# Optimization experiments

Hardware: AMD Instinct MI355X
Metric: run time of the kernel (lower is better)

## Reference

```python
import jax, jax.numpy as jnp
import numpy as np

D_MODEL = 1024
N_HEADS = 16
HEAD_DIM = D_MODEL // N_HEADS  # 64
TOP_K = 64
EPS = 1e-12  # matches F.normalize eps


def setup_inputs() -> dict:
    key = jax.random.key(0)
    ks = jax.random.split(key, 6)
    s = 0.02
    def w(k):
        return jax.random.normal(k, (D_MODEL, D_MODEL), jnp.float32) * s
    zb = jnp.zeros((D_MODEL,), jnp.float32)
    # x: (B, T, d_model); T must equal d_model (see compress_proj constraint)
    x = jax.random.normal(ks[0], (2, 1024, D_MODEL), jnp.float32)
    return {
        "x": x,
        "Wq": w(ks[1]), "bq": zb,
        "Wk": w(ks[2]), "bk": zb,
        "Wv": w(ks[3]), "bv": zb,
        "Wo": w(ks[4]), "bo": zb,
        "Wc": w(ks[5]), "bc": zb,  # compress_proj (applied along time axis)
    }


def _l2norm(a):
    n = jnp.linalg.norm(a, axis=-1, keepdims=True)
    return a / jnp.maximum(n, EPS)


def reference(x, Wq, bq, Wk, bk, Wv, bv, Wo, bo, Wc, bc):
    B, T, Dm = x.shape
    H, hd = N_HEADS, HEAD_DIM

    def proj(W, b):
        return (x @ W.T + b).reshape(B, T, H, hd).transpose(0, 2, 1, 3)  # (B,H,T,hd)

    Q = proj(Wq, bq)
    K = proj(Wk, bk)
    V = proj(Wv, bv)

    # compress_kv with compress_ratio=1: compress_proj acts on the (transposed)
    # time axis, so K_comp[b,h,c,d] = sum_t K[b,h,t,d] * Wc[c,t] + bc[c]
    K_comp = jnp.einsum('bhtd,ct->bhcd', K, Wc) + bc[None, None, :, None]
    V_comp = jnp.einsum('bhtd,ct->bhcd', V, Wc) + bc[None, None, :, None]

    # lightning indexer: cosine similarity + top-k over compressed slots
    sim = jnp.einsum('bhtd,bhcd->bhtc', _l2norm(Q), _l2norm(K_comp))
    topk_idx = jax.lax.top_k(sim, TOP_K)[1]  # (B,H,T,K)

    bi = jnp.arange(B)[:, None, None, None]
    hi = jnp.arange(H)[None, :, None, None]
    K_sel = K_comp[bi, hi, topk_idx]  # (B,H,T,K,hd)
    V_sel = V_comp[bi, hi, topk_idx]

    scores = jnp.einsum('bhtd,bhtkd->bhtk', Q, K_sel) / float(np.sqrt(hd))
    attn = jax.nn.softmax(scores, axis=-1)
    out = jnp.einsum('bhtk,bhtkd->bhtd', attn, V_sel)  # (B,H,T,hd)
    out = out.transpose(0, 2, 1, 3).reshape(B, T, Dm)
    return out @ Wo.T + bo
```

## Files before the change

kernel.cpp:

```cpp
#include <hip/hip_runtime.h>
#include <type_traits>


#define DEVI __device__ __forceinline__

constexpr int Tn = 1024;
constexpr int Cn = 1024;
constexpr int Hn = 16;

typedef short bf16x8 __attribute__((ext_vector_type(8)));
typedef float f32x4 __attribute__((ext_vector_type(4)));

DEVI int wsumi(int v)   { for (int m = 1; m < 64; m <<= 1) v += __shfl_xor(v, m); return v; }
DEVI int wmini(int v)   { for (int m = 1; m < 64; m <<= 1) { int o = __shfl_xor(v, m); v = o < v ? o : v; } return v; }
DEVI float wfmax(float v){ for (int m = 1; m < 64; m <<= 1) v = fmaxf(v, __shfl_xor(v, m)); return v; }
DEVI float wfsum(float v){ for (int m = 1; m < 64; m <<= 1) v += __shfl_xor(v, m); return v; }

DEVI unsigned long long mapd(double x) {
  unsigned long long b = (unsigned long long)__double_as_longlong(x);
  return (b >> 63) ? ~b : (b | 0x8000000000000000ull);
}

DEVI unsigned short f2bf_rne(float x) {
  unsigned u = __float_as_uint(x);
  u += 0x7fffu + ((u >> 16) & 1u);
  return (unsigned short)(u >> 16);
}
struct BfPair { short hi, lo; };
DEVI BfPair split2(float x) {
  unsigned short h = f2bf_rne(x);
  float hf = __uint_as_float(((unsigned)h) << 16);
  BfPair r;
  r.hi = (short)h;
  r.lo = (short)f2bf_rne(x - hf);
  return r;
}

template <typename OUTT, typename ACCT, bool BTRANS, int BIASMODE, bool SIM>
__global__ __launch_bounds__(256) void gemm_k(
    const float* __restrict__ A, const float* __restrict__ B,
    const float* __restrict__ bias, OUTT* __restrict__ C,
    int Kd, int lda, int ldb, int ldc,
    long long zA, long long zB, long long zC, int group_base)
{
  __shared__ float As[16][68];
  __shared__ float Bs[16][68];

  size_t offA, offB, offC;
  if (SIM) {
    int pair = group_base + (int)blockIdx.z;
    int bb = pair >> 4, hh = pair & 15;
    offA = ((size_t)bb * Tn) * (size_t)lda + (size_t)hh * 64;
    offB = ((size_t)bb * Cn) * (size_t)ldb + (size_t)hh * 64;
    offC = (size_t)blockIdx.z * (size_t)Tn * (size_t)ldc;
  } else {
    offA = (size_t)blockIdx.z * (size_t)zA;
    offB = (size_t)blockIdx.z * (size_t)zB;
    offC = (size_t)blockIdx.z * (size_t)zC;
  }
  const float* Ab = A + offA;
  const float* Bb = B + offB;
  OUTT* Cb = C + offC;

  const int tid = threadIdx.x;
  const int tx = tid & 15, ty = tid >> 4;
  const int m0 = blockIdx.y * 64, n0 = blockIdx.x * 64;

  ACCT acc[4][4];
#pragma unroll
  for (int i = 0; i < 4; ++i)
#pragma unroll
    for (int j = 0; j < 4; ++j) acc[i][j] = (ACCT)0;

  for (int k0 = 0; k0 < Kd; k0 += 16) {
    {
      int m = tid >> 2, kf = tid & 3;
      float4 a = *(const float4*)(Ab + (size_t)(m0 + m) * lda + k0 + 4 * kf);
      As[4 * kf + 0][m] = a.x; As[4 * kf + 1][m] = a.y;
      As[4 * kf + 2][m] = a.z; As[4 * kf + 3][m] = a.w;
    }
    if (BTRANS) {
      int n = tid >> 2, kf = tid & 3;
      float4 b = *(const float4*)(Bb + (size_t)(n0 + n) * ldb + k0 + 4 * kf);
      Bs[4 * kf + 0][n] = b.x; Bs[4 * kf + 1][n] = b.y;
      Bs[4 * kf + 2][n] = b.z; Bs[4 * kf + 3][n] = b.w;
    } else {
      int k = tid >> 4, nf = tid & 15;
      float4 b = *(const float4*)(Bb + (size_t)(k0 + k) * ldb + n0 + 4 * nf);
      *(float4*)&Bs[k][4 * nf] = b;
    }
    __syncthreads();
#pragma unroll
    for (int k = 0; k < 16; ++k) {
      float4 a4 = *(const float4*)&As[k][4 * ty];
      float4 b4 = *(const float4*)&Bs[k][4 * tx];
      float av[4] = {a4.x, a4.y, a4.z, a4.w};
      float bv[4] = {b4.x, b4.y, b4.z, b4.w};
#pragma unroll
      for (int i = 0; i < 4; ++i)
#pragma unroll
        for (int j = 0; j < 4; ++j)
          acc[i][j] += (ACCT)av[i] * (ACCT)bv[j];
    }
    __syncthreads();
  }

  if constexpr (std::is_same<OUTT, double>::value) {
#pragma unroll
    for (int i = 0; i < 4; ++i) {
      size_t m = (size_t)(m0 + 4 * ty + i);
      double* p = (double*)Cb + m * ldc + n0 + 4 * tx;
      p[0] = (double)acc[i][0]; p[1] = (double)acc[i][1];
      p[2] = (double)acc[i][2]; p[3] = (double)acc[i][3];
    }
  } else {
    float cbv[4] = {0.f, 0.f, 0.f, 0.f};
    if (BIASMODE == 1) {
      float4 b4 = *(const float4*)(bias + n0 + 4 * tx);
      cbv[0] = b4.x; cbv[1] = b4.y; cbv[2] = b4.z; cbv[3] = b4.w;
    }
#pragma unroll
    for (int i = 0; i < 4; ++i) {
      int m = m0 + 4 * ty + i;
      float rb = (BIASMODE == 2) ? bias[m] : 0.f;
      float4 s;
      s.x = (float)acc[i][0] + cbv[0] + rb;
      s.y = (float)acc[i][1] + cbv[1] + rb;
      s.z = (float)acc[i][2] + cbv[2] + rb;
      s.w = (float)acc[i][3] + cbv[3] + rb;
      *(float4*)((float*)Cb + (size_t)m * ldc + n0 + 4 * tx) = s;
    }
  }
}

template <bool BTRANS, int BIASMODE>
__global__ __launch_bounds__(256) void mfma_gemm_k(
    const float* __restrict__ A, const float* __restrict__ B,
    const float* __restrict__ bias, float* __restrict__ C,
    int Kd, int lda, int ldb, int ldc, long long zB, long long zC)
{
  __shared__ short Ah[4 * 64 * 8];
  __shared__ short Al[4 * 64 * 8];
  __shared__ short Bh[4 * 64 * 8];
  __shared__ short Bl[4 * 64 * 8];

  const float* Bz = B + (size_t)blockIdx.z * (size_t)zB;
  float* Cz = C + (size_t)blockIdx.z * (size_t)zC;

  const int tid = threadIdx.x;
  const int lane = tid & 63, w = tid >> 6;
  const int wr = w >> 1, wc = w & 1;
  const int m0 = blockIdx.y * 64, n0 = blockIdx.x * 64;
  const int r16 = lane & 15, kg = lane >> 4;

  f32x4 acc[2][2];
#pragma unroll
  for (int i = 0; i < 2; ++i)
#pragma unroll
    for (int j = 0; j < 2; ++j) acc[i][j] = (f32x4){0.f, 0.f, 0.f, 0.f};

  for (int k0 = 0; k0 < Kd; k0 += 32) {
    {
      int row = tid >> 2, kseg = tid & 3;
      const float* p = A + (size_t)(m0 + row) * lda + k0 + kseg * 8;
      float4 v0 = *(const float4*)p;
      float4 v1 = *(const float4*)(p + 4);
      BfPair q0 = split2(v0.x), q1 = split2(v0.y), q2 = split2(v0.z), q3 = split2(v0.w);
      BfPair q4 = split2(v1.x), q5 = split2(v1.y), q6 = split2(v1.z), q7 = split2(v1.w);
      bf16x8 h = {q0.hi, q1.hi, q2.hi, q3.hi, q4.hi, q5.hi, q6.hi, q7.hi};
      bf16x8 l = {q0.lo, q1.lo, q2.lo, q3.lo, q4.lo, q5.lo, q6.lo, q7.lo};
      int idx = (kseg * 64 + row) * 8;
      *(bf16x8*)&Ah[idx] = h;
      *(bf16x8*)&Al[idx] = l;
    }
    if (BTRANS) {
      int row = tid >> 2, kseg = tid & 3;
      const float* p = Bz + (size_t)(n0 + row) * ldb + k0 + kseg * 8;
      float4 v0 = *(const float4*)p;
      float4 v1 = *(const float4*)(p + 4);
      BfPair q0 = split2(v0.x), q1 = split2(v0.y), q2 = split2(v0.z), q3 = split2(v0.w);
      BfPair q4 = split2(v1.x), q5 = split2(v1.y), q6 = split2(v1.z), q7 = split2(v1.w);
      bf16x8 h = {q0.hi, q1.hi, q2.hi, q3.hi, q4.hi, q5.hi, q6.hi, q7.hi};
      bf16x8 l = {q0.lo, q1.lo, q2.lo, q3.lo, q4.lo, q5.lo, q6.lo, q7.lo};
      int idx = (kseg * 64 + row) * 8;
      *(bf16x8*)&Bh[idx] = h;
      *(bf16x8*)&Bl[idx] = l;
    } else {
      int col = tid & 63, kseg = tid >> 6;
      short hv[8], lv[8];
#pragma unroll
      for (int j = 0; j < 8; ++j) {
        BfPair p = split2(Bz[(size_t)(k0 + kseg * 8 + j) * ldb + n0 + col]);
        hv[j] = p.hi; lv[j] = p.lo;
      }
      bf16x8 h = {hv[0], hv[1], hv[2], hv[3], hv[4], hv[5], hv[6], hv[7]};
      bf16x8 l = {lv[0], lv[1], lv[2], lv[3], lv[4], lv[5], lv[6], lv[7]};
      int idx = (kseg * 64 + col) * 8;
      *(bf16x8*)&Bh[idx] = h;
      *(bf16x8*)&Bl[idx] = l;
    }
    __syncthreads();

    bf16x8 ah[2], al[2], bh[2], bl[2];
#pragma unroll
    for (int f = 0; f < 2; ++f) {
      int ia = (kg * 64 + wr * 32 + f * 16 + r16) * 8;
      int ib = (kg * 64 + wc * 32 + f * 16 + r16) * 8;
      ah[f] = *(const bf16x8*)&Ah[ia];
      al[f] = *(const bf16x8*)&Al[ia];
      bh[f] = *(const bf16x8*)&Bh[ib];
      bl[f] = *(const bf16x8*)&Bl[ib];
    }
#pragma unroll
    for (int fr = 0; fr < 2; ++fr)
#pragma unroll
      for (int fc = 0; fc < 2; ++fc) {
        f32x4 c = acc[fr][fc];
        c = __builtin_amdgcn_mfma_f32_16x16x32_bf16(al[fr], bh[fc], c, 0, 0, 0);
        c = __builtin_amdgcn_mfma_f32_16x16x32_bf16(ah[fr], bl[fc], c, 0, 0, 0);
        c = __builtin_amdgcn_mfma_f32_16x16x32_bf16(ah[fr], bh[fc], c, 0, 0, 0);
        acc[fr][fc] = c;
      }
    __syncthreads();
  }

#pragma unroll
  for (int fr = 0; fr < 2; ++fr)
#pragma unroll
    for (int fc = 0; fc < 2; ++fc) {
      int col = n0 + wc * 32 + fc * 16 + r16;
      float cb = (BIASMODE == 1) ? bias[col] : 0.f;
#pragma unroll
      for (int rr = 0; rr < 4; ++rr) {
        int row = m0 + wr * 32 + fr * 16 + kg * 4 + rr;
        float rb = (BIASMODE == 2) ? bias[row] : 0.f;
        Cz[(size_t)row * ldc + col] = acc[fr][fc][rr] + cb + rb;
      }
    }
}

__global__ __launch_bounds__(256) void kn_k2(const float* __restrict__ Kc,
                                             double* __restrict__ kn)
{
  int idx = (int)blockIdx.x * 256 + (int)threadIdx.x;
  int c = idx & 1023;
  int p = idx >> 10;
  int b = p >> 4, h = p & 15;
  const float* row = Kc + ((size_t)(b * 1024 + c)) * 1024 + h * 64;
  double s = 0.0;
  for (int d = 0; d < 64; ++d) { double v = (double)row[d]; s += v * v; }
  kn[(size_t)p * 1024 + c] = 1.0 / fmax(sqrt(s), 1e-12);
}

__global__ __launch_bounds__(256) void topk_attn_k(
    const double* __restrict__ dotb, const double* __restrict__ kn,
    const float* __restrict__ Vc, float* __restrict__ attnout, int group_base)
{
  __shared__ int sC[4][64];
  __shared__ float sD[4][64];

  const int lane = threadIdx.x & 63, wv = threadIdx.x >> 6;
  const int g = (int)blockIdx.x >> 8;
  const int t = ((int)blockIdx.x & 255) * 4 + wv;
  const int pair = group_base + g;
  const int bb = pair >> 4, hh = pair & 15;

  const double* drow = dotb + ((size_t)g * Tn + t) * (size_t)Cn;
  const double* knr  = kn + ((size_t)(bb * Hn + hh)) * Cn;

  double dv[16];
  unsigned long long u[16];
#pragma unroll
  for (int j = 0; j < 8; ++j) {
    double2 dd = *(const double2*)(drow + j * 128 + 2 * lane);
    double2 kk = *(const double2*)(knr  + j * 128 + 2 * lane);
    dv[2 * j] = dd.x; dv[2 * j + 1] = dd.y;
    u[2 * j]     = mapd(dd.x * kk.x);
    u[2 * j + 1] = mapd(dd.y * kk.y);
  }
  unsigned hi[16];
#pragma unroll
  for (int i = 0; i < 16; ++i) hi[i] = (unsigned)(u[i] >> 32);

  unsigned TH = 0;
  for (int bit = 31; bit >= 0; --bit) {
    unsigned Tc = TH | (1u << bit);
    int c = 0;
#pragma unroll
    for (int i = 0; i < 16; ++i) c += (hi[i] >= Tc);
    if (wsumi(c) >= 64) TH = Tc;
  }
  int mhi = 0;
#pragma unroll
  for (int i = 0; i < 16; ++i) mhi += (hi[i] > TH);
  mhi = wsumi(mhi);
  const int need1 = 64 - mhi;
  unsigned TL = 0;
  for (int bit = 31; bit >= 0; --bit) {
    unsigned Tc = TL | (1u << bit);
    int c = 0;
#pragma unroll
    for (int i = 0; i < 16; ++i) c += (hi[i] == TH && (unsigned)u[i] >= Tc);
    if (wsumi(c) >= need1) TL = Tc;
  }
  const unsigned long long V64 = ((unsigned long long)TH << 32) | TL;

  int base = 0;
#pragma unroll
  for (int i = 0; i < 16; ++i) {
    const int cix = 128 * (i >> 1) + 2 * lane + (i & 1);
    bool sel = (u[i] > V64);
    unsigned long long mk = __ballot(sel);
    if (sel) {
      int r = __popcll(mk & ((1ull << lane) - 1ull));
      sC[wv][base + r] = cix;
      sD[wv][base + r] = (float)dv[i];
    }
    base += __popcll(mk);
  }
  const int need = 64 - base;
  unsigned taken = 0;
  for (int r = 0; r < need; ++r) {
    int mn = 0x7fffffff;
#pragma unroll
    for (int i = 0; i < 16; ++i) {
      int cix = 128 * (i >> 1) + 2 * lane + (i & 1);
      if (u[i] == V64 && !((taken >> i) & 1u)) mn = mn < cix ? mn : cix;
    }
    mn = wmini(mn);
#pragma unroll
    for (int i = 0; i < 16; ++i) {
      int cix = 128 * (i >> 1) + 2 * lane + (i & 1);
      if (u[i] == V64 && !((taken >> i) & 1u) && cix == mn) {
        taken |= 1u << i;
        sC[wv][base + r] = mn;
        sD[wv][base + r] = (float)dv[i];
      }
    }
  }
  __syncthreads();

  int ck = sC[wv][lane];
  float sc = sD[wv][lane] * 0.125f;
  float mx = wfmax(sc);
  float w = expf(sc - mx);
  float sw = wfsum(w);
  w /= sw;

  const float* Vb = Vc + (size_t)bb * ((size_t)Cn * 1024) + hh * 64 + lane;
  float acc = 0.f;
#pragma unroll 4
  for (int k = 0; k < 64; ++k) {
    int c = __shfl(ck, k);
    float wk = __shfl(w, k);
    acc = fmaf(wk, Vb[(size_t)c * 1024], acc);
  }
  attnout[((size_t)(bb * Tn + t)) * 1024 + hh * 64 + lane] = acc;
}

extern "C" void kernel_launch(void* const* d_in, const int* in_sizes, int n_in,
                              void* d_out, int out_size, void* d_ws, size_t ws_size,
                              hipStream_t stream)
{
  const float* x  = (const float*)d_in[0];
  const float* Wq = (const float*)d_in[1];
  const float* bq = (const float*)d_in[2];
  const float* Wk = (const float*)d_in[3];
  const float* bk = (const float*)d_in[4];
  const float* Wv = (const float*)d_in[5];
  const float* bv = (const float*)d_in[6];
  const float* Wo = (const float*)d_in[7];
  const float* bo = (const float*)d_in[8];
  const float* Wc = (const float*)d_in[9];
  const float* bc = (const float*)d_in[10];
  float* out = (float*)d_out;

  const size_t NE = (size_t)2048 * 1024;
  float* Q  = (float*)d_ws;
  float* Kf = Q + NE;
  float* Vf = Kf + NE;
  float* Kc = Vf + NE;
  float* Vc = Kc + NE;
  float* at = Vc + NE;
  double* kn = (double*)(at + NE);
  double* tail = kn + 32768;

  const size_t fixedB = 6 * NE * 4 + 32768 * 8;
  const size_t dotPairB = (size_t)Tn * Cn * 8;
  if (ws_size < fixedB) return;

  size_t rem = ws_size - fixedB;
  double* dotp; int G;
  if      (rem >= 8 * dotPairB) { G = 8; dotp = tail; }
  else if (rem >= 4 * dotPairB) { G = 4; dotp = tail; }
  else if (rem >= 2 * dotPairB) { G = 2; dotp = tail; }
  else { G = 2; dotp = (double*)Kf; }

  dim3 blk(256, 1, 1);
  const long long M1 = 1024 * 1024;

  gemm_k<float, double, true, 1, false><<<dim3(16, 32, 1), blk, 0, stream>>>(
      x, Wq, bq, Q, 1024, 1024, 1024, 1024, 0, 0, 0, 0);
  gemm_k<float, double, true, 1, false><<<dim3(16, 32, 1), blk, 0, stream>>>(
      x, Wk, bk, Kf, 1024, 1024, 1024, 1024, 0, 0, 0, 0);
  mfma_gemm_k<true, 1><<<dim3(16, 32, 1), blk, 0, stream>>>(
      x, Wv, bv, Vf, 1024, 1024, 1024, 1024, 0, 0);

  gemm_k<float, double, false, 2, false><<<dim3(16, 16, 2), blk, 0, stream>>>(
      Wc, Kf, bc, Kc, 1024, 1024, 1024, 1024, 0, M1, M1, 0);
  mfma_gemm_k<false, 2><<<dim3(16, 16, 2), blk, 0, stream>>>(
      Wc, Vf, bc, Vc, 1024, 1024, 1024, 1024, M1, M1);

  kn_k2<<<dim3(128), dim3(256), 0, stream>>>(Kc, kn);

  for (int gb = 0; gb < 32; gb += G) {
    gemm_k<double, double, true, 0, true><<<dim3(16, 16, G), blk, 0, stream>>>(
        Q, Kc, nullptr, dotp, 64, 1024, 1024, 1024, 0, 0, 0, gb);
    topk_attn_k<<<dim3(256 * G), blk, 0, stream>>>(dotp, kn, Vc, at, gb);
  }

  mfma_gemm_k<true, 1><<<dim3(16, 32, 1), blk, 0, stream>>>(
      at, Wo, bo, out, 1024, 1024, 1024, 1024, 0, 0);
}
```

Before: 962.2 us.

## Pre-split operands into packed bf16 hi/lo and halve FP64 GEMM tile height

Adds a presplit kernel that converts fp32 operands into packed bf16 hi/lo pairs once. A new MFMA GEMM reads these packed pairs instead of splitting fp32 values inside every tile. The V projection, V compression, attention output and output projection now produce or consume the packed format, which removes repeated conversion work. The double-precision GEMMs use 32-row tiles so the grids double and occupancy rises. The similarity/top-k loop is fixed at 2 pairs per launch with the dot buffer aliased onto Kf, which drops the larger-group option and adds extra presplit launches.

```diff
diff --git a/kernel.cpp b/kernel.cpp
--- a/kernel.cpp
+++ b/kernel.cpp
@@ -35,18 +35,24 @@
   r.lo = (short)f2bf_rne(x - hf);
   return r;
 }
+DEVI unsigned packbf(float x) {
+  BfPair p = split2(x);
+  return ((unsigned)(unsigned short)p.hi << 16) | (unsigned)(unsigned short)p.lo;
+}
+DEVI short uhi(unsigned u) { return (short)(u >> 16); }
+DEVI short ulo(unsigned u) { return (short)(u & 0xffffu); }
 
 template <typename OUTT, typename ACCT, bool BTRANS, int BIASMODE, bool SIM>
-__global__ __launch_bounds__(256) void gemm_k(
+__global__ __launch_bounds__(256) void gemm32_k(
     const float* __restrict__ A, const float* __restrict__ B,
     const float* __restrict__ bias, OUTT* __restrict__ C,
     int Kd, int lda, int ldb, int ldc,
-    long long zA, long long zB, long long zC, int group_base)
-{
-  __shared__ float As[16][68];
+    long long zB, long long zC, int group_base)
+{
+  __shared__ float As[16][34];
   __shared__ float Bs[16][68];
 
-  size_t offA, offB, offC;
+  size_t offA = 0, offB, offC;
   if (SIM) {
     int pair = group_base + (int)blockIdx.z;
     int bb = pair >> 4, hh = pair & 15;
@@ -54,7 +60,6 @@
     offB = ((size_t)bb * Cn) * (size_t)ldb + (size_t)hh * 64;
     offC = (size_t)blockIdx.z * (size_t)Tn * (size_t)ldc;
   } else {
-    offA = (size_t)blockIdx.z * (size_t)zA;
     offB = (size_t)blockIdx.z * (size_t)zB;
     offC = (size_t)blockIdx.z * (size_t)zC;
   }
@@ -64,16 +69,16 @@
 
   const int tid = threadIdx.x;
   const int tx = tid & 15, ty = tid >> 4;
-  const int m0 = blockIdx.y * 64, n0 = blockIdx.x * 64;
-
-  ACCT acc[4][4];
-#pragma unroll
-  for (int i = 0; i < 4; ++i)
+  const int m0 = blockIdx.y * 32, n0 = blockIdx.x * 64;
+
+  ACCT acc[2][4];
+#pragma unroll
+  for (int i = 0; i < 2; ++i)
 #pragma unroll
     for (int j = 0; j < 4; ++j) acc[i][j] = (ACCT)0;
 
   for (int k0 = 0; k0 < Kd; k0 += 16) {
-    {
+    if (tid < 128) {
       int m = tid >> 2, kf = tid & 3;
       float4 a = *(const float4*)(Ab + (size_t)(m0 + m) * lda + k0 + 4 * kf);
       As[4 * kf + 0][m] = a.x; As[4 * kf + 1][m] = a.y;
@@ -92,12 +97,12 @@
     __syncthreads();
 #pragma unroll
     for (int k = 0; k < 16; ++k) {
-      float4 a4 = *(const float4*)&As[k][4 * ty];
+      float2 a2 = *(const float2*)&As[k][2 * ty];
       float4 b4 = *(const float4*)&Bs[k][4 * tx];
-      float av[4] = {a4.x, a4.y, a4.z, a4.w};
+      float av[2] = {a2.x, a2.y};
       float bv[4] = {b4.x, b4.y, b4.z, b4.w};
 #pragma unroll
-      for (int i = 0; i < 4; ++i)
+      for (int i = 0; i < 2; ++i)
 #pragma unroll
         for (int j = 0; j < 4; ++j)
           acc[i][j] += (ACCT)av[i] * (ACCT)bv[j];
@@ -107,8 +112,8 @@
 
   if constexpr (std::is_same<OUTT, double>::value) {
 #pragma unroll
-    for (int i = 0; i < 4; ++i) {
-      size_t m = (size_t)(m0 + 4 * ty + i);
+    for (int i = 0; i < 2; ++i) {
+      size_t m = (size_t)(m0 + 2 * ty + i);
       double* p = (double*)Cb + m * ldc + n0 + 4 * tx;
       p[0] = (double)acc[i][0]; p[1] = (double)acc[i][1];
       p[2] = (double)acc[i][2]; p[3] = (double)acc[i][3];
@@ -120,8 +125,8 @@
       cbv[0] = b4.x; cbv[1] = b4.y; cbv[2] = b4.z; cbv[3] = b4.w;
     }
 #pragma unroll
-    for (int i = 0; i < 4; ++i) {
-      int m = m0 + 4 * ty + i;
+    for (int i = 0; i < 2; ++i) {
+      int m = m0 + 2 * ty + i;
       float rb = (BIASMODE == 2) ? bias[m] : 0.f;
       float4 s;
       s.x = (float)acc[i][0] + cbv[0] + rb;
@@ -131,6 +136,126 @@
       *(float4*)((float*)Cb + (size_t)m * ldc + n0 + 4 * tx) = s;
     }
   }
+}
+
+__global__ __launch_bounds__(256) void presplit_k(const float* __restrict__ src,
+                                                  unsigned* __restrict__ dst, int n4)
+{
+  int stride = (int)gridDim.x * 256;
+  for (int i = (int)blockIdx.x * 256 + (int)threadIdx.x; i < n4; i += stride) {
+    float4 v = ((const float4*)src)[i];
+    uint4 o;
+    o.x = packbf(v.x); o.y = packbf(v.y); o.z = packbf(v.z); o.w = packbf(v.w);
+    ((uint4*)dst)[i] = o;
+  }
+}
+
+template <bool BTRANS, int BIASMODE, bool OUTPACK>
+__global__ __launch_bounds__(256) void mfma_ps_k(
+    const unsigned* __restrict__ A, const unsigned* __restrict__ B,
+    const float* __restrict__ bias, void* __restrict__ Cv,
+    int Kd, int lda, int ldb, int ldc, long long zB, long long zC)
+{
+  __shared__ short Ah[4 * 64 * 8];
+  __shared__ short Al[4 * 64 * 8];
+  __shared__ short Bh[4 * 64 * 8];
+  __shared__ short Bl[4 * 64 * 8];
+
+  const unsigned* Bz = B + (size_t)blockIdx.z * (size_t)zB;
+
+  const int tid = threadIdx.x;
+  const int lane = tid & 63, w = tid >> 6;
+  const int wr = w >> 1, wc = w & 1;
+  const int m0 = blockIdx.y * 64, n0 = blockIdx.x * 64;
+  const int r16 = lane & 15, kg = lane >> 4;
+
+  f32x4 acc[2][2];
+#pragma unroll
+  for (int i = 0; i < 2; ++i)
+#pragma unroll
+    for (int j = 0; j < 2; ++j) acc[i][j] = (f32x4){0.f, 0.f, 0.f, 0.f};
+
+  for (int k0 = 0; k0 < Kd; k0 += 32) {
+    {
+      int row = tid >> 2, kseg = tid & 3;
+      const unsigned* pa = A + (size_t)(m0 + row) * lda + k0 + kseg * 8;
+      uint4 u0 = *(const uint4*)pa;
+      uint4 u1 = *(const uint4*)(pa + 4);
+      bf16x8 h = {uhi(u0.x), uhi(u0.y), uhi(u0.z), uhi(u0.w),
+                  uhi(u1.x), uhi(u1.y), uhi(u1.z), uhi(u1.w)};
+      bf16x8 l = {ulo(u0.x), ulo(u0.y), ulo(u0.z), ulo(u0.w),
+                  ulo(u1.x), ulo(u1.y), ulo(u1.z), ulo(u1.w)};
+      int idx = (kseg * 64 + row) * 8;
+      *(bf16x8*)&Ah[idx] = h;
+      *(bf16x8*)&Al[idx] = l;
+    }
+    if (BTRANS) {
+      int row = tid >> 2, kseg = tid & 3;
+      const unsigned* pb = Bz + (size_t)(n0 + row) * ldb + k0 + kseg * 8;
+      uint4 u0 = *(const uint4*)pb;
+      uint4 u1 = *(const uint4*)(pb + 4);
+      bf16x8 h = {uhi(u0.x), uhi(u0.y), uhi(u0.z), uhi(u0.w),
+                  uhi(u1.x), uhi(u1.y), uhi(u1.z), uhi(u1.w)};
+      bf16x8 l = {ulo(u0.x), ulo(u0.y), ulo(u0.z), ulo(u0.w),
+                  ulo(u1.x), ulo(u1.y), ulo(u1.z), ulo(u1.w)};
+      int idx = (kseg * 64 + row) * 8;
+      *(bf16x8*)&Bh[idx] = h;
+      *(bf16x8*)&Bl[idx] = l;
+    } else {
+      int col = tid & 63, kseg = tid >> 6;
+      short hv[8], lv[8];
+#pragma unroll
+      for (int j = 0; j < 8; ++j) {
+        unsigned u = Bz[(size_t)(k0 + kseg * 8 + j) * ldb + n0 + col];
+        hv[j] = uhi(u); lv[j] = ulo(u);
+      }
+      bf16x8 h = {hv[0], hv[1], hv[2], hv[3], hv[4], hv[5], hv[6], hv[7]};
+      bf16x8 l = {lv[0], lv[1], lv[2], lv[3], lv[4], lv[5], lv[6], lv[7]};
+      int idx = (kseg * 64 + col) * 8;
+      *(bf16x8*)&Bh[idx] = h;
+      *(bf16x8*)&Bl[idx] = l;
+    }
+    __syncthreads();
+
+    bf16x8 ah[2], al[2], bh[2], bl[2];
+#pragma unroll
+    for (int f = 0; f < 2; ++f) {
+      int ia = (kg * 64 + wr * 32 + f * 16 + r16) * 8;
+      int ib = (kg * 64 + wc * 32 + f * 16 + r16) * 8;
+      ah[f] = *(const bf16x8*)&Ah[ia];
+      al[f] = *(const bf16x8*)&Al[ia];
+      bh[f] = *(const bf16x8*)&Bh[ib];
+      bl[f] = *(const bf16x8*)&Bl[ib];
+    }
+#pragma unroll
+    for (int fr = 0; fr < 2; ++fr)
+#pragma unroll
+      for (int fc = 0; fc < 2; ++fc) {
+        f32x4 c = acc[fr][fc];
+        c = __builtin_amdgcn_mfma_f32_16x16x32_bf16(al[fr], bh[fc], c, 0, 0, 0);
+        c = __builtin_amdgcn_mfma_f32_16x16x32_bf16(ah[fr], bl[fc], c, 0, 0, 0);
+        c = __builtin_amdgcn_mfma_f32_16x16x32_bf16(ah[fr], bh[fc], c, 0, 0, 0);
+        acc[fr][fc] = c;
+      }
+    __syncthreads();
+  }
+
+#pragma unroll
+  for (int fr = 0; fr < 2; ++fr)
+#pragma unroll
+    for (int fc = 0; fc < 2; ++fc) {
+      int col = n0 + wc * 32 + fc * 16 + r16;
+      float cb = (BIASMODE == 1) ? bias[col] : 0.f;
+#pragma unroll
+      for (int rr = 0; rr < 4; ++rr) {
+        int row = m0 + wr * 32 + fr * 16 + kg * 4 + rr;
+        float rb = (BIASMODE == 2) ? bias[row] : 0.f;
+        float v = acc[fr][fc][rr] + cb + rb;
+        size_t o = (size_t)row * ldc + col + (size_t)blockIdx.z * (size_t)zC;
+        if (OUTPACK) ((unsigned*)Cv)[o] = packbf(v);
+        else         ((float*)Cv)[o] = v;
+      }
+    }
 }
 
 template <bool BTRANS, int BIASMODE>
@@ -252,9 +377,10 @@
   kn[(size_t)p * 1024 + c] = 1.0 / fmax(sqrt(s), 1e-12);
 }
 
+template <bool PACK>
 __global__ __launch_bounds__(256) void topk_attn_k(
     const double* __restrict__ dotb, const double* __restrict__ kn,
-    const float* __restrict__ Vc, float* __restrict__ attnout, int group_base)
+    const float* __restrict__ Vc, void* __restrict__ atOut, int group_base)
 {
   __shared__ int sC[4][64];
   __shared__ float sD[4][64];
@@ -355,7 +481,9 @@
     float wk = __shfl(w, k);
     acc = fmaf(wk, Vb[(size_t)c * 1024], acc);
   }
-  attnout[((size_t)(bb * Tn + t)) * 1024 + hh * 64 + lane] = acc;
+  size_t o = ((size_t)(bb * Tn + t)) * 1024 + hh * 64 + lane;
+  if (PACK) ((unsigned*)atOut)[o] = packbf(acc);
+  else      ((float*)atOut)[o] = acc;
 }
 
 extern "C" void kernel_launch(void* const* d_in, const int* in_sizes, int n_in,
@@ -376,49 +504,69 @@
   float* out = (float*)d_out;
 
   const size_t NE = (size_t)2048 * 1024;
-  float* Q  = (float*)d_ws;
-  float* Kf = Q + NE;
-  float* Vf = Kf + NE;
-  float* Kc = Vf + NE;
-  float* Vc = Kc + NE;
-  float* at = Vc + NE;
+  float* Q   = (float*)d_ws;
+  float* Kf  = Q + NE;
+  float* Vf  = Kf + NE;
+  float* Kc  = Vf + NE;
+  float* Vc  = Kc + NE;
+  float* at  = Vc + NE;
   double* kn = (double*)(at + NE);
-  double* tail = kn + 32768;
+  unsigned* Wspl = (unsigned*)(kn + 32768);
+
+  unsigned* xs_ats = (unsigned*)at;
+  unsigned* Vfs    = (unsigned*)Vf;
+  double* dotp = (double*)Kf;
 
   const size_t fixedB = 6 * NE * 4 + 32768 * 8;
-  const size_t dotPairB = (size_t)Tn * Cn * 8;
   if (ws_size < fixedB) return;
-
-  size_t rem = ws_size - fixedB;
-  double* dotp; int G;
-  if      (rem >= 8 * dotPairB) { G = 8; dotp = tail; }
-  else if (rem >= 4 * dotPairB) { G = 4; dotp = tail; }
-  else if (rem >= 2 * dotPairB) { G = 2; dotp = tail; }
-  else { G = 2; dotp = (double*)Kf; }
+  const bool TA = ws_size >= fixedB + ((size_t)1 << 22);
 
   dim3 blk(256, 1, 1);
   const long long M1 = 1024 * 1024;
 
-  gemm_k<float, double, true, 1, false><<<dim3(16, 32, 1), blk, 0, stream>>>(
-      x, Wq, bq, Q, 1024, 1024, 1024, 1024, 0, 0, 0, 0);
-  gemm_k<float, double, true, 1, false><<<dim3(16, 32, 1), blk, 0, stream>>>(
-      x, Wk, bk, Kf, 1024, 1024, 1024, 1024, 0, 0, 0, 0);
-  mfma_gemm_k<true, 1><<<dim3(16, 32, 1), blk, 0, stream>>>(
-      x, Wv, bv, Vf, 1024, 1024, 1024, 1024, 0, 0);
-
-  gemm_k<float, double, false, 2, false><<<dim3(16, 16, 2), blk, 0, stream>>>(
-      Wc, Kf, bc, Kc, 1024, 1024, 1024, 1024, 0, M1, M1, 0);
-  mfma_gemm_k<false, 2><<<dim3(16, 16, 2), blk, 0, stream>>>(
-      Wc, Vf, bc, Vc, 1024, 1024, 1024, 1024, M1, M1);
-
-  kn_k2<<<dim3(128), dim3(256), 0, stream>>>(Kc, kn);
-
-  for (int gb = 0; gb < 32; gb += G) {
-    gemm_k<double, double, true, 0, true><<<dim3(16, 16, G), blk, 0, stream>>>(
-        Q, Kc, nullptr, dotp, 64, 1024, 1024, 1024, 0, 0, 0, gb);
-    topk_attn_k<<<dim3(256 * G), blk, 0, stream>>>(dotp, kn, Vc, at, gb);
-  }
-
-  mfma_gemm_k<true, 1><<<dim3(16, 32, 1), blk, 0, stream>>>(
-      at, Wo, bo, out, 1024, 1024, 1024, 1024, 0, 0);
-}
+  gemm32_k<float, double, true, 1, false><<<dim3(16, 64, 1), blk, 0, stream>>>(
+      x, Wq, bq, Q, 1024, 1024, 1024, 1024, 0, 0, 0);
+  gemm32_k<float, double, true, 1, false><<<dim3(16, 64, 1), blk, 0, stream>>>(
+      x, Wk, bk, Kf, 1024, 1024, 1024, 1024, 0, 0, 0);
+
+  if (TA) {
+    presplit_k<<<dim3(512), blk, 0, stream>>>(x, xs_ats, (int)(NE / 4));
+    presplit_k<<<dim3(512), blk, 0, stream>>>(Wv, Wspl, (int)(M1 / 4));
+    mfma_ps_k<true, 1, true><<<dim3(16, 32, 1), blk, 0, stream>>>(
+        xs_ats, Wspl, bv, Vfs, 1024, 1024, 1024, 1024, 0, 0);
+  } else {
+    mfma_gemm_k<true, 1><<<dim3(16, 32, 1), blk, 0, stream>>>(
+        x, Wv, bv, Vf, 1024, 1024, 1024, 1024, 0, 0);
+  }
+
+  gemm32_k<float, double, false, 2, false><<<dim3(16, 32, 2), blk, 0, stream>>>(
+      Wc, Kf, bc, Kc, 1024, 1024, 1024, 1024, M1, M1, 0);
+  if (TA) {
+    presplit_k<<<dim3(512), blk, 0, stream>>>(Wc, Wspl, (int)(M1 / 4));
+    mfma_ps_k<false, 2, false><<<dim3(16, 16, 2), blk, 0, stream>>>(
+        Wspl, Vfs, bc, Vc, 1024, 1024, 1024, 1024, M1, M1);
+  } else {
+    mfma_gemm_k<false, 2><<<dim3(16, 16, 2), blk, 0, stream>>>(
+        Wc, Vf, bc, Vc, 1024, 1024, 1024, 1024, M1, M1);
+  }
+
+  kn_k2<<<dim3(128), blk, 0, stream>>>(Kc, kn);
+
+  for (int gb = 0; gb < 32; gb += 2) {
+    gemm32_k<double, double, true, 0, true><<<dim3(16, 32, 2), blk, 0, stream>>>(
+        Q, Kc, nullptr, dotp, 64, 1024, 1024, 1024, 0, 0, gb);
+    if (TA)
+      topk_attn_k<true><<<dim3(512), blk, 0, stream>>>(dotp, kn, Vc, xs_ats, gb);
+    else
+      topk_attn_k<false><<<dim3(512), blk, 0, stream>>>(dotp, kn, Vc, at, gb);
+  }
+
+  if (TA) {
+    presplit_k<<<dim3(512), blk, 0, stream>>>(Wo, Wspl, (int)(M1 / 4));
+    mfma_ps_k<true, 1, false><<<dim3(16, 32, 1), blk, 0, stream>>>(
+        xs_ats, Wspl, bo, out, 1024, 1024, 1024, 1024, 0, 0);
+  } else {
+    mfma_gemm_k<true, 1><<<dim3(16, 32, 1), blk, 0, stream>>>(
+        at, Wo, bo, out, 1024, 1024, 1024, 1024, 0, 0);
+  }
+}
```

Measured after the change: 1.353 ms. 40.6% more time.
